# Performance work log

Measured on AMD Instinct MI355X. Metric: run time of the kernel, lower is better.

## Reference

```python
import jax, jax.numpy as jnp
import numpy as np

N_NODES = 100000
N_EDGES = 640000
IN_FEATS = 256
HEADS = 4
OUT_FEATS = 32
NEG_SLOPE = 0.2


def setup_inputs() -> dict:
    key = jax.random.key(0)
    k_feat, k_src, k_dst, k_w, k_al, k_ar = jax.random.split(key, 6)
    feat = jax.random.normal(k_feat, (N_NODES, IN_FEATS), dtype=jnp.float32)
    src = jax.random.randint(k_src, (N_EDGES,), 0, N_NODES, dtype=jnp.int32)
    dst = jax.random.randint(k_dst, (N_EDGES,), 0, N_NODES, dtype=jnp.int32)
    # fc: Linear(in_feats, out_feats*num_heads, bias=False); store as [in, H*D]
    W = jax.random.normal(k_w, (IN_FEATS, HEADS * OUT_FEATS), dtype=jnp.float32) * 0.05
    attn_l = jax.random.normal(k_al, (HEADS, OUT_FEATS), dtype=jnp.float32) * 0.1
    attn_r = jax.random.normal(k_ar, (HEADS, OUT_FEATS), dtype=jnp.float32) * 0.1
    return {"feat": feat, "W": W, "attn_l": attn_l, "attn_r": attn_r, "src": src, "dst": dst}


def reference(feat, W, attn_l, attn_r, src, dst):
    N = feat.shape[0]
    H, D = attn_l.shape
    # fc + reshape to [N, H, D]
    ft = (feat @ W).reshape(N, H, D)
    # per-node attention logits [N, H]
    el = jnp.einsum('nhd,hd->nh', ft, attn_l)
    er = jnp.einsum('nhd,hd->nh', ft, attn_r)
    # u_add_v then leaky relu -> per-edge logits [E, H]
    e = el[src] + er[dst]
    e = jnp.where(e > 0, e, NEG_SLOPE * e)
    # edge softmax over incoming edges of each dst node (per head)
    m = jax.ops.segment_max(e, dst, num_segments=N)  # [N, H]
    m = jnp.where(jnp.isfinite(m), m, jnp.zeros_like(m))  # empty segments
    ex = jnp.exp(e - m[dst])
    denom = jax.ops.segment_sum(ex, dst, num_segments=N)  # [N, H]
    a = ex / denom[dst]  # [E, H]
    # u_mul_e + sum aggregation: rst[v] = sum_{(u,v)} a_uv * ft[u]
    msg = ft[src] * a[:, :, None]  # [E, H, D]
    rst = jax.ops.segment_sum(msg, dst, num_segments=N)  # [N, H, D]
    return rst, a[:, :, None]
```

## Files before the change

kernel.cpp:

```cpp
#include <hip/hip_runtime.h>
#include <hip/hip_bf16.h>

#define N_NODES 100000
#define N_EDGES 640000
#define IN_F 256
#define HD 128
#define BM 64

using f32x4 = __attribute__((ext_vector_type(4))) float;
using s8v   = __attribute__((ext_vector_type(8))) short;

__device__ __forceinline__ short bf16rn(float x) {
  unsigned u = __builtin_bit_cast(unsigned, x);
  return (short)((u + 0x7FFFu + ((u >> 16) & 1u)) >> 16);
}
__device__ __forceinline__ float bf16tof(short h) {
  unsigned u = ((unsigned)(unsigned short)h) << 16;
  return __builtin_bit_cast(float, u);
}

typedef const __attribute__((address_space(1))) void gvoid;
typedef __attribute__((address_space(3))) void lvoid;
__device__ __forceinline__ void gl_lds16(const void* g, char* l) {
  __builtin_amdgcn_global_load_lds((gvoid*)g, (lvoid*)l, 16, 0, 0);
}

__global__ __launch_bounds__(256) void prep_b(const float* __restrict__ W,
                                              short* __restrict__ Bth)
{
  int c = blockIdx.x;
  int k = threadIdx.x;
  Bth[(size_t)c * IN_F + k] = bf16rn(W[(size_t)k * HD + c]);
}

__global__ __launch_bounds__(256) void prep_x(const float* __restrict__ W,
    const float* __restrict__ al, const float* __restrict__ ar,
    short* __restrict__ Bxh)
{
  int c = blockIdx.x;
  int k = threadIdx.x;
  float v = 0.f;
  if (c < 8) {
    int h = c & 3;
    const float* att = (c < 4) ? al : ar;
    #pragma unroll
    for (int d = 0; d < 32; d++)
      v += W[(size_t)k * HD + h * 32 + d] * att[h * 32 + d];
  }
  Bxh[(size_t)c * IN_F + k] = bf16rn(v);
}

__device__ __forceinline__ void stage_tile(char* lds, int wid, int lane, int kt,
    const float* feat, const short* Bth, const short* Bxh, int rb, int M)
{
  const int k0 = kt * 32;
  char* Ab = lds + (kt & 1) * 8192;
  char* Bb = lds + 16384 + (kt & 1) * 8192;
  char* Xb = lds + 32768 + (kt & 1) * 1024;
  int gr = rb + lane; if (gr > M - 1) gr = M - 1;
  #pragma unroll
  for (int s = 0; s < 4; s++) {
    const int o = wid + s * 4;
    if (o < 8) {
      gl_lds16(feat + (size_t)gr * IN_F + k0 + o * 4, Ab + o * 1024);
    } else {
      int j = o - 8;
      int c = (j & 1) * 64 + lane, lg = j >> 1;
      gl_lds16(Bth + (size_t)c * IN_F + k0 + lg * 8, Bb + j * 1024);
    }
  }
  if (wid == 0) {
    int c = lane & 15, lg = lane >> 4;
    gl_lds16(Bxh + (size_t)c * IN_F + k0 + lg * 8, Xb);
  }
}

__global__ __launch_bounds__(256) void gemm_mfma(const float* __restrict__ feat,
    const short* __restrict__ Bth, const short* __restrict__ Bxh,
    float* __restrict__ ft, float* __restrict__ el, float* __restrict__ er, int M)
{
  __shared__ char lds[34816];
  const int wid  = threadIdx.x >> 6;
  const int lane = threadIdx.x & 63;
  const int lr = lane & 15;
  const int lg = lane >> 4;
  const int wm = (wid >> 1) * 32;
  const int wn = (wid & 1) * 64;
  const int rb = blockIdx.x * BM;
  const bool doX = (wid & 1) == 0;

  f32x4 acc[2][4];
  f32x4 accx[2];
  #pragma unroll
  for (int mi = 0; mi < 2; mi++) {
    accx[mi] = (f32x4){0.f, 0.f, 0.f, 0.f};
    #pragma unroll
    for (int ni = 0; ni < 4; ni++) acc[mi][ni] = (f32x4){0.f, 0.f, 0.f, 0.f};
  }

  stage_tile(lds, wid, lane, 0, feat, Bth, Bxh, rb, M);
  __syncthreads();

  #pragma unroll
  for (int kt = 0; kt < 8; ++kt) {
    if (kt < 7) stage_tile(lds, wid, lane, kt + 1, feat, Bth, Bxh, rb, M);

    const char* Ab = lds + (kt & 1) * 8192;
    const char* Bb = lds + 16384 + (kt & 1) * 8192;
    const char* Xb = lds + 32768 + (kt & 1) * 1024;

    s8v Bf[4];
    #pragma unroll
    for (int ni = 0; ni < 4; ni++)
      Bf[ni] = *(const s8v*)(Bb + (((lg << 7) + wn + ni * 16 + lr) << 4));
    s8v Xf = *(const s8v*)(Xb + (((lg << 4) + lr) << 4));

    #pragma unroll
    for (int mi = 0; mi < 2; mi++) {
      const int row = wm + mi * 16 + lr;
      const float4 a0 = *(const float4*)(Ab + ((((lg * 2 + 0) << 6) + row) << 4));
      const float4 a1 = *(const float4*)(Ab + ((((lg * 2 + 1) << 6) + row) << 4));
      const float av[8] = {a0.x, a0.y, a0.z, a0.w, a1.x, a1.y, a1.z, a1.w};
      s8v ah, alo;
      #pragma unroll
      for (int j = 0; j < 8; j++) {
        short h = bf16rn(av[j]);
        ah[j]  = h;
        alo[j] = bf16rn(av[j] - bf16tof(h));
      }
      #pragma unroll
      for (int ni = 0; ni < 4; ni++) {
        acc[mi][ni] = __builtin_amdgcn_mfma_f32_16x16x32_bf16(ah,  Bf[ni], acc[mi][ni], 0, 0, 0);
        acc[mi][ni] = __builtin_amdgcn_mfma_f32_16x16x32_bf16(alo, Bf[ni], acc[mi][ni], 0, 0, 0);
      }
      if (doX) {
        accx[mi] = __builtin_amdgcn_mfma_f32_16x16x32_bf16(ah,  Xf, accx[mi], 0, 0, 0);
        accx[mi] = __builtin_amdgcn_mfma_f32_16x16x32_bf16(alo, Xf, accx[mi], 0, 0, 0);
      }
    }
    __syncthreads();
  }

  #pragma unroll
  for (int mi = 0; mi < 2; mi++) {
    int rbase = rb + wm + mi * 16 + lg * 4;
    #pragma unroll
    for (int ni = 0; ni < 4; ni++) {
      int col = wn + ni * 16 + lr;
      #pragma unroll
      for (int r = 0; r < 4; r++) {
        int grow = rbase + r;
        if (grow < M) ft[(size_t)grow * HD + col] = acc[mi][ni][r];
      }
    }
    if (doX) {
      #pragma unroll
      for (int r = 0; r < 4; r++) {
        int grow = rbase + r;
        if (grow < M) {
          if (lr < 4)      el[(size_t)grow * 4 + lr]       = accx[mi][r];
          else if (lr < 8) er[(size_t)grow * 4 + (lr - 4)] = accx[mi][r];
        }
      }
    }
  }
}

__global__ void deg_kernel(const int* __restrict__ dst, int* __restrict__ deg) {
  int i = blockIdx.x * blockDim.x + threadIdx.x;
  if (i < N_EDGES) atomicAdd(&deg[dst[i]], 1);
}

__global__ __launch_bounds__(256) void scanA(const int* __restrict__ deg,
    int* __restrict__ excl, int* __restrict__ partials, int n)
{
  __shared__ int s[256];
  int t = threadIdx.x;
  int base = blockIdx.x * 1024 + t * 4;
  int d0 = (base + 0 < n) ? deg[base + 0] : 0;
  int d1 = (base + 1 < n) ? deg[base + 1] : 0;
  int d2 = (base + 2 < n) ? deg[base + 2] : 0;
  int d3 = (base + 3 < n) ? deg[base + 3] : 0;
  int sum = d0 + d1 + d2 + d3;
  s[t] = sum; __syncthreads();
  for (int off = 1; off < 256; off <<= 1) {
    int x = 0; if (t >= off) x = s[t - off];
    __syncthreads(); s[t] += x; __syncthreads();
  }
  int e0 = s[t] - sum;
  if (base + 0 < n) excl[base + 0] = e0;
  if (base + 1 < n) excl[base + 1] = e0 + d0;
  if (base + 2 < n) excl[base + 2] = e0 + d0 + d1;
  if (base + 3 < n) excl[base + 3] = e0 + d0 + d1 + d2;
  if (t == 255) partials[blockIdx.x] = s[255];
}

__global__ void scanB(int* partials, int nb) {
  __shared__ int s[128];
  int t = threadIdx.x;
  int v = (t < nb) ? partials[t] : 0;
  s[t] = v; __syncthreads();
  for (int off = 1; off < 128; off <<= 1) {
    int x = 0; if (t >= off) x = s[t - off];
    __syncthreads(); s[t] += x; __syncthreads();
  }
  if (t < nb) partials[t] = s[t] - v;
}

__global__ __launch_bounds__(256) void scanC(int* __restrict__ row_ptr,
    const int* __restrict__ partials, int n, int E)
{
  int t = threadIdx.x;
  int base = blockIdx.x * 1024 + t * 4;
  int add = partials[blockIdx.x];
  #pragma unroll
  for (int j = 0; j < 4; j++) if (base + j < n) row_ptr[base + j] += add;
  if (blockIdx.x == 0 && t == 0) row_ptr[n] = E;
}

__global__ void scatter_kernel(const int* __restrict__ src, const int* __restrict__ dst,
                               const int* __restrict__ row_ptr,
                               int* __restrict__ cursor, int* __restrict__ usrc) {
  int e = blockIdx.x * blockDim.x + threadIdx.x;
  if (e >= N_EDGES) return;
  int d = dst[e];
  int pos = row_ptr[d] + atomicAdd(&cursor[d], 1);
  usrc[pos] = src[e];
}

__global__ __launch_bounds__(256) void gat_node(const int* __restrict__ row_ptr,
    const int* __restrict__ usrc,
    const float* __restrict__ el, const float* __restrict__ er4,
    const float* __restrict__ ft, float* __restrict__ rst,
    float* __restrict__ lse, int n)
{
  __shared__ int   su[4][64];
  __shared__ float sex[4][64][4];
  const int w = threadIdx.x >> 6;
  const int lane = threadIdx.x & 63;
  const int v = blockIdx.x * 4 + w;
  if (v >= n) return;
  const int s0 = row_ptr[v];
  const int d  = row_ptr[v + 1] - s0;
  const int g  = lane >> 4;

  if (d == 0) {
    *(float2*)(rst + (size_t)v * HD + 2 * lane) = make_float2(0.f, 0.f);
    return;
  }

  const float4 erv = *(const float4*)(er4 + (size_t)v * 4);
  float m0 = -1e30f, m1 = -1e30f, m2 = -1e30f, m3 = -1e30f;
  float den = 0.f;
  float2 acc = make_float2(0.f, 0.f);

  for (int c0 = 0; c0 < d; c0 += 64) {
    const int cd = min(64, d - c0);
    float x0 = -1e30f, x1 = -1e30f, x2 = -1e30f, x3 = -1e30f;
    int u = 0;
    if (lane < cd) {
      u = usrc[s0 + c0 + lane];
      const float4 elv = *(const float4*)(el + (size_t)u * 4);
      x0 = elv.x + erv.x; x0 = x0 > 0.f ? x0 : 0.2f * x0;
      x1 = elv.y + erv.y; x1 = x1 > 0.f ? x1 : 0.2f * x1;
      x2 = elv.z + erv.z; x2 = x2 > 0.f ? x2 : 0.2f * x2;
      x3 = elv.w + erv.w; x3 = x3 > 0.f ? x3 : 0.2f * x3;
    }
    su[w][lane] = u;
    float n0 = x0, n1 = x1, n2 = x2, n3 = x3;
    #pragma unroll
    for (int off = 32; off >= 1; off >>= 1) {
      n0 = fmaxf(n0, __shfl_xor(n0, off));
      n1 = fmaxf(n1, __shfl_xor(n1, off));
      n2 = fmaxf(n2, __shfl_xor(n2, off));
      n3 = fmaxf(n3, __shfl_xor(n3, off));
    }
    n0 = fmaxf(n0, m0); n1 = fmaxf(n1, m1); n2 = fmaxf(n2, m2); n3 = fmaxf(n3, m3);
    float e0 = __expf(x0 - n0), e1 = __expf(x1 - n1);
    float e2 = __expf(x2 - n2), e3 = __expf(x3 - n3);
    sex[w][lane][0] = e0; sex[w][lane][1] = e1;
    sex[w][lane][2] = e2; sex[w][lane][3] = e3;
    float mg = g == 0 ? m0 : g == 1 ? m1 : g == 2 ? m2 : m3;
    float ng = g == 0 ? n0 : g == 1 ? n1 : g == 2 ? n2 : n3;
    float scale = __expf(mg - ng);
    den *= scale; acc.x *= scale; acc.y *= scale;
    m0 = n0; m1 = n1; m2 = n2; m3 = n3;
    asm volatile("s_waitcnt lgkmcnt(0)" ::: "memory");
    #pragma unroll 4
    for (int j = 0; j < cd; ++j) {
      int uu = su[w][j];
      float wgt = sex[w][j][g];
      float2 f = *(const float2*)(ft + (size_t)uu * HD + 2 * lane);
      den += wgt;
      acc.x += wgt * f.x; acc.y += wgt * f.y;
    }
  }
  *(float2*)(rst + (size_t)v * HD + 2 * lane) = make_float2(acc.x / den, acc.y / den);
  if ((lane & 15) == 0) {
    float mg = g == 0 ? m0 : g == 1 ? m1 : g == 2 ? m2 : m3;
    lse[(size_t)v * 4 + g] = mg + __logf(den);
  }
}

__global__ void norm_kernel(const int* __restrict__ src, const int* __restrict__ dst,
                            const float* __restrict__ el, const float* __restrict__ er,
                            const float* __restrict__ lse, float* __restrict__ a, int E)
{
  int i = blockIdx.x * blockDim.x + threadIdx.x;
  if (i >= E) return;
  int u = src[i], v = dst[i];
  const float4 elv = *(const float4*)(el + (size_t)u * 4);
  const float4 erv = *(const float4*)(er + (size_t)v * 4);
  const float4 ls  = *(const float4*)(lse + (size_t)v * 4);
  float x0 = elv.x + erv.x; x0 = x0 > 0.f ? x0 : 0.2f * x0;
  float x1 = elv.y + erv.y; x1 = x1 > 0.f ? x1 : 0.2f * x1;
  float x2 = elv.z + erv.z; x2 = x2 > 0.f ? x2 : 0.2f * x2;
  float x3 = elv.w + erv.w; x3 = x3 > 0.f ? x3 : 0.2f * x3;
  float4 o;
  o.x = __expf(x0 - ls.x); o.y = __expf(x1 - ls.y);
  o.z = __expf(x2 - ls.z); o.w = __expf(x3 - ls.w);
  *(float4*)(a + (size_t)i * 4) = o;
}

extern "C" void kernel_launch(void* const* d_in, const int* in_sizes, int n_in,
                              void* d_out, int out_size, void* d_ws, size_t ws_size,
                              hipStream_t stream)
{
  const float* feat = (const float*)d_in[0];
  const float* W    = (const float*)d_in[1];
  const float* al   = (const float*)d_in[2];
  const float* ar   = (const float*)d_in[3];
  const int*   src  = (const int*)d_in[4];
  const int*   dst  = (const int*)d_in[5];
  float* rst   = (float*)d_out;
  float* a_out = rst + (size_t)N_NODES * HD;

  char* w = (char*)d_ws;
  auto alloc = [&](size_t bytes) { char* p = w; w += (bytes + 255) & ~(size_t)255; return p; };
  float* ft      = (float*)alloc((size_t)N_NODES * HD * 4);
  float* el      = (float*)alloc((size_t)N_NODES * 4 * 4);
  float* er      = (float*)alloc((size_t)N_NODES * 4 * 4);
  float* lse     = (float*)alloc((size_t)N_NODES * 4 * 4);
  int*   deg     = (int*)alloc((size_t)N_NODES * 4);
  int*   row_ptr = (int*)alloc(((size_t)N_NODES + 1) * 4);
  int*   cursor  = (int*)alloc((size_t)N_NODES * 4);
  int*   partials= (int*)alloc(1024);
  int*   usrc    = (int*)alloc((size_t)N_EDGES * 4);
  short* Bth     = (short*)alloc((size_t)HD * IN_F * 2);
  short* Bxh     = (short*)alloc((size_t)16 * IN_F * 2);

  hipMemsetAsync(deg, 0, N_NODES * 4, stream);
  hipMemsetAsync(cursor, 0, N_NODES * 4, stream);

  prep_b<<<128, 256, 0, stream>>>(W, Bth);
  prep_x<<<16, 256, 0, stream>>>(W, al, ar, Bxh);
  gemm_mfma<<<(N_NODES + BM - 1) / BM, 256, 0, stream>>>(feat, Bth, Bxh, ft, el, er, N_NODES);
  deg_kernel<<<(N_EDGES + 255) / 256, 256, 0, stream>>>(dst, deg);
  scanA<<<98, 256, 0, stream>>>(deg, row_ptr, partials, N_NODES);
  scanB<<<1, 128, 0, stream>>>(partials, 98);
  scanC<<<98, 256, 0, stream>>>(row_ptr, partials, N_NODES, N_EDGES);
  scatter_kernel<<<(N_EDGES + 255) / 256, 256, 0, stream>>>(src, dst, row_ptr, cursor, usrc);
  gat_node<<<(N_NODES + 3) / 4, 256, 0, stream>>>(row_ptr, usrc, el, er, ft, rst, lse, N_NODES);
  norm_kernel<<<(N_EDGES + 255) / 256, 256, 0, stream>>>(src, dst, el, er, lse, a_out, N_EDGES);
}
```

Baseline: 353.5 us.

## Stage full A tile once in swizzled LDS, read pre-permuted B from global

The GEMM kernel now loads the whole 64x256 fp32 A tile into 64KB of LDS in one shot, using an XOR swizzle to avoid bank conflicts, instead of double-buffering 32-wide k slices. The weight matrices are pre-permuted by the prep kernels into the MFMA fragment order and read straight from global/L2 rather than staged through LDS. This removes the per-k-step barriers. The larger LDS footprint lowers occupancy, and B fragments now come from global memory in the inner loop.

```diff
diff --git a/kernel.cpp b/kernel.cpp
--- a/kernel.cpp
+++ b/kernel.cpp
@@ -26,16 +26,17 @@
 }
 
 __global__ __launch_bounds__(256) void prep_b(const float* __restrict__ W,
-                                              short* __restrict__ Bth)
+                                              short* __restrict__ Btp)
 {
   int c = blockIdx.x;
   int k = threadIdx.x;
-  Bth[(size_t)c * IN_F + k] = bf16rn(W[(size_t)k * HD + c]);
+  int kt = k >> 5, lg = (k >> 3) & 3, j = k & 7;
+  Btp[(((size_t)(kt * 4 + lg) * 128 + c) << 3) + j] = bf16rn(W[(size_t)k * HD + c]);
 }
 
 __global__ __launch_bounds__(256) void prep_x(const float* __restrict__ W,
     const float* __restrict__ al, const float* __restrict__ ar,
-    short* __restrict__ Bxh)
+    short* __restrict__ Xp)
 {
   int c = blockIdx.x;
   int k = threadIdx.x;
@@ -47,39 +48,26 @@
     for (int d = 0; d < 32; d++)
       v += W[(size_t)k * HD + h * 32 + d] * att[h * 32 + d];
   }
-  Bxh[(size_t)c * IN_F + k] = bf16rn(v);
-}
-
-__device__ __forceinline__ void stage_tile(char* lds, int wid, int lane, int kt,
-    const float* feat, const short* Bth, const short* Bxh, int rb, int M)
-{
-  const int k0 = kt * 32;
-  char* Ab = lds + (kt & 1) * 8192;
-  char* Bb = lds + 16384 + (kt & 1) * 8192;
-  char* Xb = lds + 32768 + (kt & 1) * 1024;
-  int gr = rb + lane; if (gr > M - 1) gr = M - 1;
+  int kt = k >> 5, lg = (k >> 3) & 3, j = k & 7;
+  Xp[(((size_t)kt * 64 + lg * 16 + c) << 3) + j] = bf16rn(v);
+}
+
+__device__ __forceinline__ void stage_A(char* Asm, int wid, int lane,
+                                        const float* feat, int rb, int M)
+{
   #pragma unroll
-  for (int s = 0; s < 4; s++) {
+  for (int s = 0; s < 16; s++) {
     const int o = wid + s * 4;
-    if (o < 8) {
-      gl_lds16(feat + (size_t)gr * IN_F + k0 + o * 4, Ab + o * 1024);
-    } else {
-      int j = o - 8;
-      int c = (j & 1) * 64 + lane, lg = j >> 1;
-      gl_lds16(Bth + (size_t)c * IN_F + k0 + lg * 8, Bb + j * 1024);
-    }
-  }
-  if (wid == 0) {
-    int c = lane & 15, lg = lane >> 4;
-    gl_lds16(Bxh + (size_t)c * IN_F + k0 + lg * 8, Xb);
+    int gr = rb + o; if (gr > M - 1) gr = M - 1;
+    gl_lds16(feat + (size_t)gr * IN_F + ((lane ^ (o & 7)) << 2), Asm + o * 1024);
   }
 }
 
 __global__ __launch_bounds__(256) void gemm_mfma(const float* __restrict__ feat,
-    const short* __restrict__ Bth, const short* __restrict__ Bxh,
+    const short* __restrict__ Btp, const short* __restrict__ Xp,
     float* __restrict__ ft, float* __restrict__ el, float* __restrict__ er, int M)
 {
-  __shared__ char lds[34816];
+  __shared__ __align__(16) char lds[65536];
   const int wid  = threadIdx.x >> 6;
   const int lane = threadIdx.x & 63;
   const int lr = lane & 15;
@@ -98,28 +86,23 @@
     for (int ni = 0; ni < 4; ni++) acc[mi][ni] = (f32x4){0.f, 0.f, 0.f, 0.f};
   }
 
-  stage_tile(lds, wid, lane, 0, feat, Bth, Bxh, rb, M);
+  stage_A(lds, wid, lane, feat, rb, M);
   __syncthreads();
 
-  #pragma unroll
+  #pragma unroll 4
   for (int kt = 0; kt < 8; ++kt) {
-    if (kt < 7) stage_tile(lds, wid, lane, kt + 1, feat, Bth, Bxh, rb, M);
-
-    const char* Ab = lds + (kt & 1) * 8192;
-    const char* Bb = lds + 16384 + (kt & 1) * 8192;
-    const char* Xb = lds + 32768 + (kt & 1) * 1024;
-
     s8v Bf[4];
     #pragma unroll
     for (int ni = 0; ni < 4; ni++)
-      Bf[ni] = *(const s8v*)(Bb + (((lg << 7) + wn + ni * 16 + lr) << 4));
-    s8v Xf = *(const s8v*)(Xb + (((lg << 4) + lr) << 4));
+      Bf[ni] = *(const s8v*)(Btp + (((size_t)(kt * 4 + lg) * 128 + wn + ni * 16 + lr) << 3));
+    s8v Xf = *(const s8v*)(Xp + (((size_t)kt * 64 + lg * 16 + lr) << 3));
 
     #pragma unroll
     for (int mi = 0; mi < 2; mi++) {
-      const int row = wm + mi * 16 + lr;
-      const float4 a0 = *(const float4*)(Ab + ((((lg * 2 + 0) << 6) + row) << 4));
-      const float4 a1 = *(const float4*)(Ab + ((((lg * 2 + 1) << 6) + row) << 4));
+      const int R = wm + mi * 16 + lr;
+      const int cb = kt * 8 + lg * 2;
+      const float4 a0 = *(const float4*)(lds + R * 1024 + (((cb + 0) ^ (R & 7)) << 4));
+      const float4 a1 = *(const float4*)(lds + R * 1024 + (((cb + 1) ^ (R & 7)) << 4));
       const float av[8] = {a0.x, a0.y, a0.z, a0.w, a1.x, a1.y, a1.z, a1.w};
       s8v ah, alo;
       #pragma unroll
@@ -138,7 +121,6 @@
         accx[mi] = __builtin_amdgcn_mfma_f32_16x16x32_bf16(alo, Xf, accx[mi], 0, 0, 0);
       }
     }
-    __syncthreads();
   }
 
   #pragma unroll
@@ -346,15 +328,15 @@
   int*   cursor  = (int*)alloc((size_t)N_NODES * 4);
   int*   partials= (int*)alloc(1024);
   int*   usrc    = (int*)alloc((size_t)N_EDGES * 4);
-  short* Bth     = (short*)alloc((size_t)HD * IN_F * 2);
-  short* Bxh     = (short*)alloc((size_t)16 * IN_F * 2);
+  short* Btp     = (short*)alloc((size_t)HD * IN_F * 2);
+  short* Xp      = (short*)alloc((size_t)16 * IN_F * 2);
 
   hipMemsetAsync(deg, 0, N_NODES * 4, stream);
   hipMemsetAsync(cursor, 0, N_NODES * 4, stream);
 
-  prep_b<<<128, 256, 0, stream>>>(W, Bth);
-  prep_x<<<16, 256, 0, stream>>>(W, al, ar, Bxh);
-  gemm_mfma<<<(N_NODES + BM - 1) / BM, 256, 0, stream>>>(feat, Bth, Bxh, ft, el, er, N_NODES);
+  prep_b<<<128, 256, 0, stream>>>(W, Btp);
+  prep_x<<<16, 256, 0, stream>>>(W, al, ar, Xp);
+  gemm_mfma<<<(N_NODES + BM - 1) / BM, 256, 0, stream>>>(feat, Btp, Xp, ft, el, er, N_NODES);
   deg_kernel<<<(N_EDGES + 255) / 256, 256, 0, stream>>>(dst, deg);
   scanA<<<98, 256, 0, stream>>>(deg, row_ptr, partials, N_NODES);
   scanB<<<1, 128, 0, stream>>>(partials, 98);
```

Measured after the change: 351.2 us. Within noise of the previous version (-0.6%).
